# Performance work log

Hardware: AMD Instinct MI355X
Metric: run time of the kernel (lower is better)

Reference implementation:

```python
import jax, jax.numpy as jnp
import numpy as np

VOCAB = 33
V2 = VOCAB * VOCAB  # 1089
BUCKETS = 512


def setup_inputs() -> dict:
    key = jax.random.key(0)
    ks = jax.random.split(key, 9)
    B, S = 4096, 4096
    src = jax.random.randint(ks[0], (B, S), 0, VOCAB, dtype=jnp.int64 if jax.config.jax_enable_x64 else jnp.int32)
    def lin(k, fan_in, fan_out):
        bound = 1.0 / np.sqrt(fan_in)
        return jax.random.uniform(k, (fan_in, fan_out), jnp.float32, -bound, bound)
    return {
        "src": src,
        "Wb1": lin(ks[1], V2, 256), "bb1": jax.random.normal(ks[2], (256,), jnp.float32) * 0.01,
        "Wb2": lin(ks[3], 256, 32), "bb2": jax.random.normal(ks[4], (32,), jnp.float32) * 0.01,
        "Wt1": lin(ks[5], BUCKETS, 256), "bt1": jax.random.normal(ks[6], (256,), jnp.float32) * 0.01,
        "Wt2": lin(ks[7], 256, 32), "bt2": jax.random.normal(ks[8], (32,), jnp.float32) * 0.01,
    }


def _hist_freqs(indices, mask, n_bins):
    # indices: [B, L] int, mask: [B, L] bool -> normalized per-row histogram [B, n_bins]
    B = indices.shape[0]
    rows = jnp.arange(B)[:, None]
    counts = jnp.zeros((B, n_bins), jnp.float32).at[rows, indices].add(mask.astype(jnp.float32))
    lens = jnp.clip(mask.sum(axis=1, keepdims=True).astype(jnp.float32), 1.0, None)
    return counts / lens


def reference(src, Wb1, bb1, Wb2, bb2, Wt1, bt1, Wt2, bt2):
    # bigram histogram
    cur, nxt = src[:, :-1], src[:, 1:]
    bi_idx = cur * VOCAB + nxt
    bi_mask = (cur > 0) & (nxt > 0)
    bi_freq = _hist_freqs(bi_idx, bi_mask, V2)
    bi_feat = jax.nn.relu(bi_freq @ Wb1 + bb1) @ Wb2 + bb2
    # trigram hashed histogram
    c1, c2, c3 = src[:, :-2], src[:, 1:-1], src[:, 2:]
    tri_idx = (c1 * (VOCAB * VOCAB) + c2 * VOCAB + c3) % BUCKETS
    tri_mask = (c1 > 0) & (c2 > 0) & (c3 > 0)
    tri_freq = _hist_freqs(tri_idx, tri_mask, BUCKETS)
    tri_feat = jax.nn.relu(tri_freq @ Wt1 + bt1) @ Wt2 + bt2
    return jnp.concatenate([bi_feat, tri_feat], axis=1)  # [B, 64]
```

## Files before the change

### kernel.cpp

```cpp
#include <hip/hip_runtime.h>
#include <hip/hip_bf16.h>

#define TOK_S    4096
#define NBI      1089
#define NBI_P    1092
#define KP_BI    1120
#define NTRI     512
#define NTRI_P   544
#define NHID     256
#define NROWS    4096
#define HSTRIDE  (NHID + 4)

#define HIST_BLKS   (NROWS / 2)
#define TRANS_ELEMS (NHID * KP_BI + NHID * NTRI)
#define TRANS_BLKS  (TRANS_ELEMS / 1024)

typedef __attribute__((ext_vector_type(8))) short short8;
typedef __attribute__((ext_vector_type(4))) float f32x4;

static __device__ __forceinline__ unsigned int f2bf(float f) {
    __hip_bfloat16 h = __float2bfloat16(f);
    return (unsigned int)*reinterpret_cast<unsigned short*>(&h);
}

__global__ __launch_bounds__(256, 4)
void hist_trans(const int* __restrict__ src,
                const float* __restrict__ Wb1, const float* __restrict__ Wt1,
                __hip_bfloat16* __restrict__ Abi,
                __hip_bfloat16* __restrict__ Atri,
                __hip_bfloat16* __restrict__ WbT,
                __hip_bfloat16* __restrict__ WtT,
                float* __restrict__ inv)
{
    __shared__ int   s_bi [2][NBI_P];
    __shared__ int   s_tri[2][NTRI_P];
    __shared__ float s_ps [2][2][2];

    const int tid = threadIdx.x;

    if (blockIdx.x >= HIST_BLKS) {
        int base = (blockIdx.x - HIST_BLKS) * 1024 + tid;
        const int nb = NHID * KP_BI;
        #pragma unroll
        for (int i = 0; i < 4; ++i) {
            int idx = base + i * 256;
            if (idx < nb) {
                int c = idx / KP_BI, k = idx - c * KP_BI;
                WbT[idx] = __float2bfloat16(k < NBI ? Wb1[k * NHID + c] : 0.0f);
            } else {
                int j = idx - nb;
                int c = j >> 9, k = j & 511;
                WtT[j] = __float2bfloat16(Wt1[k * NHID + c]);
            }
        }
        return;
    }

    const int wave = tid >> 6;
    const int lane = tid & 63;
    const int wrow = wave >> 1;
    const int wpar = wave & 1;
    const size_t row = (size_t)blockIdx.x * 2 + wrow;
    const int dump = NTRI + (lane & 31);

    for (int i = tid; i < 2 * NBI_P / 4;  i += 256) ((int4*)s_bi)[i]  = int4{0,0,0,0};
    for (int i = tid; i < 2 * NTRI_P / 4; i += 256) ((int4*)s_tri)[i] = int4{0,0,0,0};
    __syncthreads();

    int* bi  = s_bi[wrow];
    int* tri = s_tri[wrow];
    const int4* rowp = (const int4*)(src + row * TOK_S);
    const int*  rowt = src + row * TOK_S;

    int4 A[4], Bv[4];
    int2 E[4];
    #pragma unroll
    for (int jj = 0; jj < 4; ++jj) {
        const int idx = wpar * 256 + jj * 64 + lane;
        A[jj]  = rowp[2 * idx];
        Bv[jj] = rowp[2 * idx + 1];
        if (idx != 511) E[jj] = *(const int2*)(rowt + 8 * idx + 8);
        else            E[jj] = int2{0, 0};
    }

    #pragma unroll
    for (int jj = 0; jj < 4; ++jj) {
        const int t0 = A[jj].x, t1 = A[jj].y, t2 = A[jj].z, t3 = A[jj].w;
        const int t4 = Bv[jj].x, t5 = Bv[jj].y, t6 = Bv[jj].z, t7 = Bv[jj].w;
        const int t8 = E[jj].x, t9 = E[jj].y;
        const int b0 = t0 * 33 + t1;
        const int b1 = t1 * 33 + t2;
        const int b2 = t2 * 33 + t3;
        const int b3 = t3 * 33 + t4;
        const int b4 = t4 * 33 + t5;
        const int b5 = t5 * 33 + t6;
        const int b6 = t6 * 33 + t7;
        const int b7 = t7 * 33 + t8;
        atomicAdd(&bi[b0], 1);  atomicAdd(&bi[b1], 1);
        atomicAdd(&bi[b2], 1);  atomicAdd(&bi[b3], 1);
        atomicAdd(&bi[b4], 1);  atomicAdd(&bi[b5], 1);
        atomicAdd(&bi[b6], 1);  atomicAdd(&bi[b7], 1);
        const int u0 = (min(min(t0, t1), t2) > 0) ? ((b0 * 33 + t2) & 511) : dump;
        const int u1 = (min(min(t1, t2), t3) > 0) ? ((b1 * 33 + t3) & 511) : dump;
        const int u2 = (min(min(t2, t3), t4) > 0) ? ((b2 * 33 + t4) & 511) : dump;
        const int u3 = (min(min(t3, t4), t5) > 0) ? ((b3 * 33 + t5) & 511) : dump;
        const int u4 = (min(min(t4, t5), t6) > 0) ? ((b4 * 33 + t6) & 511) : dump;
        const int u5 = (min(min(t5, t6), t7) > 0) ? ((b5 * 33 + t7) & 511) : dump;
        const int u6 = (min(min(t6, t7), t8) > 0) ? ((b6 * 33 + t8) & 511) : dump;
        const int u7 = (min(min(t7, t8), t9) > 0) ? ((b7 * 33 + t9) & 511) : dump;
        atomicAdd(&tri[u0], 1); atomicAdd(&tri[u1], 1);
        atomicAdd(&tri[u2], 1); atomicAdd(&tri[u3], 1);
        atomicAdd(&tri[u4], 1); atomicAdd(&tri[u5], 1);
        atomicAdd(&tri[u6], 1); atomicAdd(&tri[u7], 1);
    }
    __syncthreads();

    float bsum = 0.0f, tsum = 0.0f;
    __hip_bfloat16* arow = Abi + row * KP_BI;
    for (int g = wpar * 64 + lane; g < KP_BI / 4; g += 128) {
        uint2 pk{0, 0};
        if (g < NBI_P / 4) {
            int4 v = *(const int4*)&bi[4 * g];
            float f0, f1, f2, f3;
            int b = 4 * g;
            f0 = (b + 0 >= 33 && (b + 0) % 33 != 0 && b + 0 < NBI) ? (float)v.x : 0.0f;
            f1 = (b + 1 >= 33 && (b + 1) % 33 != 0 && b + 1 < NBI) ? (float)v.y : 0.0f;
            f2 = (b + 2 >= 33 && (b + 2) % 33 != 0 && b + 2 < NBI) ? (float)v.z : 0.0f;
            f3 = (b + 3 >= 33 && (b + 3) % 33 != 0 && b + 3 < NBI) ? (float)v.w : 0.0f;
            bsum += f0 + f1 + f2 + f3;
            pk.x = f2bf(f0) | (f2bf(f1) << 16);
            pk.y = f2bf(f2) | (f2bf(f3) << 16);
        }
        *(uint2*)(arow + 4 * g) = pk;
    }
    {
        const int g = wpar * 64 + lane;
        int4 v = *(const int4*)&tri[4 * g];
        float f0 = (float)v.x, f1 = (float)v.y, f2 = (float)v.z, f3 = (float)v.w;
        tsum += f0 + f1 + f2 + f3;
        uint2 pk;
        pk.x = f2bf(f0) | (f2bf(f1) << 16);
        pk.y = f2bf(f2) | (f2bf(f3) << 16);
        *(uint2*)(Atri + row * NTRI + 4 * g) = pk;
    }
    #pragma unroll
    for (int s = 32; s; s >>= 1) {
        bsum += __shfl_xor(bsum, s, 64);
        tsum += __shfl_xor(tsum, s, 64);
    }
    if (lane == 0) { s_ps[wrow][wpar][0] = bsum; s_ps[wrow][wpar][1] = tsum; }
    __syncthreads();
    if (tid < 2) {
        float bs = s_ps[tid][0][0] + s_ps[tid][1][0];
        float ts = s_ps[tid][0][1] + s_ps[tid][1][1];
        size_t r2 = ((size_t)blockIdx.x * 2 + tid) * 2;
        inv[r2 + 0] = 1.0f / fmaxf(bs, 1.0f);
        inv[r2 + 1] = 1.0f / fmaxf(ts, 1.0f);
    }
}

template<int KP>
__device__ __forceinline__
void head_body(const __hip_bfloat16* __restrict__ A,
               const __hip_bfloat16* __restrict__ WT,
               const float* __restrict__ b1,
               const float* __restrict__ W2,
               const float* __restrict__ b2,
               const float* __restrict__ inv, const int invoff, const int headoff,
               float* __restrict__ out, const int m0,
               float (*sH)[HSTRIDE])
{
    const int wave = threadIdx.x >> 6;
    const int lane = threadIdx.x & 63;
    const int wn   = wave * 32;
    const int fr   = lane & 15;
    const int kg   = lane >> 4;

    const __hip_bfloat16* A0 = A  + (size_t)(m0 + fr) * KP + kg * 8;
    const __hip_bfloat16* A1 = A0 + (size_t)16 * KP;
    const __hip_bfloat16* B0 = WT + (size_t)(wn + fr) * KP + kg * 8;
    const __hip_bfloat16* B1 = B0 + (size_t)16 * KP;

    f32x4 acc00 = {}, acc01 = {}, acc10 = {}, acc11 = {};
    #pragma unroll 4
    for (int k = 0; k < KP; k += 32) {
        short8 a0  = *(const short8*)(A0 + k);
        short8 a1  = *(const short8*)(A1 + k);
        short8 b0  = *(const short8*)(B0 + k);
        short8 b1v = *(const short8*)(B1 + k);
        acc00 = __builtin_amdgcn_mfma_f32_16x16x32_bf16(a0, b0,  acc00, 0, 0, 0);
        acc01 = __builtin_amdgcn_mfma_f32_16x16x32_bf16(a0, b1v, acc01, 0, 0, 0);
        acc10 = __builtin_amdgcn_mfma_f32_16x16x32_bf16(a1, b0,  acc10, 0, 0, 0);
        acc11 = __builtin_amdgcn_mfma_f32_16x16x32_bf16(a1, b1v, acc11, 0, 0, 0);
    }

    f32x4 accs[2][2] = { {acc00, acc01}, {acc10, acc11} };
    #pragma unroll
    for (int mf = 0; mf < 2; ++mf) {
        #pragma unroll
        for (int nf = 0; nf < 2; ++nf) {
            const int col = wn + nf * 16 + fr;
            const float bias = b1[col];
            #pragma unroll
            for (int r = 0; r < 4; ++r) {
                const int rl = mf * 16 + kg * 4 + r;
                const float iv = inv[(m0 + rl) * 2 + invoff];
                sH[rl][col] = fmaxf(fmaf(accs[mf][nf][r], iv, bias), 0.0f);
            }
        }
    }
    __syncthreads();

    const int r  = threadIdx.x >> 4;
    const int oo = threadIdx.x & 15;
    const float* hr = sH[r];
    float a0 = b2[oo], a1 = b2[oo + 16];
    #pragma unroll 8
    for (int j = 0; j < NHID; j += 4) {
        float4 h = *(const float4*)(hr + j);
        a0 = fmaf(h.x, W2[(j + 0) * 32 + oo], a0);
        a0 = fmaf(h.y, W2[(j + 1) * 32 + oo], a0);
        a0 = fmaf(h.z, W2[(j + 2) * 32 + oo], a0);
        a0 = fmaf(h.w, W2[(j + 3) * 32 + oo], a0);
        a1 = fmaf(h.x, W2[(j + 0) * 32 + oo + 16], a1);
        a1 = fmaf(h.y, W2[(j + 1) * 32 + oo + 16], a1);
        a1 = fmaf(h.z, W2[(j + 2) * 32 + oo + 16], a1);
        a1 = fmaf(h.w, W2[(j + 3) * 32 + oo + 16], a1);
    }
    const size_t ro = (size_t)(m0 + r) * 64 + headoff;
    out[ro + oo]      = a0;
    out[ro + oo + 16] = a1;
}

__global__ __launch_bounds__(512, 1)
void gemm_fused(const __hip_bfloat16* __restrict__ Abi,
                const __hip_bfloat16* __restrict__ WbT,
                const float* __restrict__ bb1,
                const float* __restrict__ Wb2, const float* __restrict__ bb2,
                const __hip_bfloat16* __restrict__ Atri,
                const __hip_bfloat16* __restrict__ WtT,
                const float* __restrict__ bt1,
                const float* __restrict__ Wt2, const float* __restrict__ bt2,
                const float* __restrict__ inv,
                float* __restrict__ out)
{
    __shared__ float sH[32][HSTRIDE];
    const int bid = (blockIdx.x & 7) * 32 + (blockIdx.x >> 3);
    if (bid < NROWS / 32) {
        head_body<KP_BI>(Abi, WbT, bb1, Wb2, bb2, inv, 0, 0,  out, bid * 32, sH);
    } else {
        head_body<NTRI>(Atri, WtT, bt1, Wt2, bt2, inv, 1, 32, out, (bid - NROWS / 32) * 32, sH);
    }
}

extern "C" void kernel_launch(void* const* d_in, const int* in_sizes, int n_in,
                              void* d_out, int out_size, void* d_ws, size_t ws_size,
                              hipStream_t stream) {
    const int*   src = (const int*)  d_in[0];
    const float* Wb1 = (const float*)d_in[1];
    const float* bb1 = (const float*)d_in[2];
    const float* Wb2 = (const float*)d_in[3];
    const float* bb2 = (const float*)d_in[4];
    const float* Wt1 = (const float*)d_in[5];
    const float* bt1 = (const float*)d_in[6];
    const float* Wt2 = (const float*)d_in[7];
    const float* bt2 = (const float*)d_in[8];
    float* outp = (float*)d_out;

    const int B = in_sizes[0] / TOK_S;

    char* ws = (char*)d_ws;
    __hip_bfloat16* Abi  = (__hip_bfloat16*)(ws);
    __hip_bfloat16* Atri = (__hip_bfloat16*)(ws + (size_t)B * KP_BI * 2);
    char* ws2 = ws + (size_t)B * KP_BI * 2 + (size_t)B * NTRI * 2;
    __hip_bfloat16* WbT  = (__hip_bfloat16*)(ws2);
    __hip_bfloat16* WtT  = (__hip_bfloat16*)(ws2 + (size_t)NHID * KP_BI * 2);
    float* inv = (float*)(ws2 + (size_t)NHID * KP_BI * 2 + (size_t)NHID * NTRI * 2);

    hist_trans<<<HIST_BLKS + TRANS_BLKS, 256, 0, stream>>>(
        src, Wb1, Wt1, Abi, Atri, WbT, WtT, inv);

    gemm_fused<<<2 * (B / 32), 512, 0, stream>>>(
        Abi, WbT, bb1, Wb2, bb2, Atri, WtT, bt1, Wt2, bt2, inv, outp);
}
```

Measured before the change: 49.71 us.

## Fuse histogram and GEMM heads into one cooperative kernel with grid sync

Replaces the two-kernel pipeline (histogram/weight-transpose, then fused GEMM) with a single cooperative launch of 512 blocks of 512 threads. Each block transposes a slice of the weights, builds histograms for 8 rows in two passes, then does a grid-wide sync before computing 16-row MLP heads with MFMA. The aim is to remove the second launch and its inter-kernel gap. The cost is a grid barrier, a fixed grid shape tied to B=4096, and a smaller 16-row GEMM tile with less reuse. It falls back to the old kernels if the cooperative launch fails.

```diff
diff --git a/kernel.cpp b/kernel.cpp
--- a/kernel.cpp
+++ b/kernel.cpp
@@ -1,5 +1,8 @@
 #include <hip/hip_runtime.h>
 #include <hip/hip_bf16.h>
+#include <hip/hip_cooperative_groups.h>
+
+namespace cg = cooperative_groups;
 
 #define TOK_S    4096
 #define NBI      1089
@@ -15,12 +18,227 @@
 #define TRANS_ELEMS (NHID * KP_BI + NHID * NTRI)
 #define TRANS_BLKS  (TRANS_ELEMS / 1024)
 
+#define CGRID   512
+#define CBLK    512
+
 typedef __attribute__((ext_vector_type(8))) short short8;
 typedef __attribute__((ext_vector_type(4))) float f32x4;
 
 static __device__ __forceinline__ unsigned int f2bf(float f) {
     __hip_bfloat16 h = __float2bfloat16(f);
     return (unsigned int)*reinterpret_cast<unsigned short*>(&h);
+}
+
+struct HistLds {
+    int   bi [4][1100];
+    int   tri[4][548];
+    float ps [4][2][2];
+};
+struct GemmLds {
+    float sH[16][260];
+};
+union SharedU { HistLds h; GemmLds g; };
+
+template<int KP>
+__device__ __forceinline__
+void head16(const __hip_bfloat16* __restrict__ A,
+            const __hip_bfloat16* __restrict__ WT,
+            const float* __restrict__ b1, const float* __restrict__ W2,
+            const float* __restrict__ b2, const float* __restrict__ inv,
+            const int invoff, const int headoff,
+            float* __restrict__ out, const int m0, float (*sH)[260])
+{
+    const int tid  = threadIdx.x;
+    const int wave = tid >> 6, lane = tid & 63;
+    const int wn   = wave * 32;
+    const int fr   = lane & 15, kg = lane >> 4;
+
+    const __hip_bfloat16* Ap = A  + (size_t)(m0 + fr) * KP + kg * 8;
+    const __hip_bfloat16* B0 = WT + (size_t)(wn + fr) * KP + kg * 8;
+    const __hip_bfloat16* B1 = B0 + (size_t)16 * KP;
+
+    f32x4 acc0 = {}, acc1 = {};
+    #pragma unroll 4
+    for (int k = 0; k < KP; k += 32) {
+        short8 a   = *(const short8*)(Ap + k);
+        short8 b0  = *(const short8*)(B0 + k);
+        short8 b1v = *(const short8*)(B1 + k);
+        acc0 = __builtin_amdgcn_mfma_f32_16x16x32_bf16(a, b0,  acc0, 0, 0, 0);
+        acc1 = __builtin_amdgcn_mfma_f32_16x16x32_bf16(a, b1v, acc1, 0, 0, 0);
+    }
+
+    #pragma unroll
+    for (int nf = 0; nf < 2; ++nf) {
+        const f32x4 acc = nf ? acc1 : acc0;
+        const int col = wn + nf * 16 + fr;
+        const float bias = b1[col];
+        #pragma unroll
+        for (int r = 0; r < 4; ++r) {
+            const int rl = kg * 4 + r;
+            const float iv = inv[(m0 + rl) * 2 + invoff];
+            sH[rl][col] = fmaxf(fmaf(acc[r], iv, bias), 0.0f);
+        }
+    }
+    __syncthreads();
+
+    const int rr = tid >> 5, o = tid & 31;
+    const float* hr = sH[rr];
+    float a0 = b2[o];
+    #pragma unroll 8
+    for (int j = 0; j < NHID; j += 4) {
+        float4 h = *(const float4*)(hr + j);
+        a0 = fmaf(h.x, W2[(j + 0) * 32 + o], a0);
+        a0 = fmaf(h.y, W2[(j + 1) * 32 + o], a0);
+        a0 = fmaf(h.z, W2[(j + 2) * 32 + o], a0);
+        a0 = fmaf(h.w, W2[(j + 3) * 32 + o], a0);
+    }
+    out[(size_t)(m0 + rr) * 64 + headoff + o] = a0;
+}
+
+__global__ __launch_bounds__(CBLK, 4)
+void ngram_coop(const int* __restrict__ src,
+                const float* __restrict__ Wb1, const float* __restrict__ Wt1,
+                const float* __restrict__ bb1, const float* __restrict__ Wb2,
+                const float* __restrict__ bb2, const float* __restrict__ bt1,
+                const float* __restrict__ Wt2, const float* __restrict__ bt2,
+                __hip_bfloat16* __restrict__ Abi, __hip_bfloat16* __restrict__ Atri,
+                __hip_bfloat16* __restrict__ WbT, __hip_bfloat16* __restrict__ WtT,
+                float* __restrict__ inv, float* __restrict__ out)
+{
+    cg::grid_group grid = cg::this_grid();
+    __shared__ __align__(16) SharedU u;
+
+    const int tid  = threadIdx.x;
+    const int bid  = blockIdx.x;
+    const int wave = tid >> 6, lane = tid & 63;
+    const int wrow = wave >> 1, wpar = wave & 1;
+
+    {
+        const int nb = NHID * KP_BI;
+        #pragma unroll
+        for (int it = 0; it < 2; ++it) {
+            const int t = tid + it * 512;
+            if (t < 816) {
+                int idx = bid * 816 + t;
+                if (idx < nb) {
+                    int c = idx / KP_BI, k = idx - c * KP_BI;
+                    WbT[idx] = __float2bfloat16(k < NBI ? Wb1[k * NHID + c] : 0.0f);
+                } else {
+                    int j = idx - nb;
+                    int c = j >> 9, k = j & 511;
+                    WtT[j] = __float2bfloat16(Wt1[k * NHID + c]);
+                }
+            }
+        }
+    }
+
+    const int dump = NTRI + (lane & 31);
+    for (int pass = 0; pass < 2; ++pass) {
+        const int4 z{0, 0, 0, 0};
+        for (int i = tid; i < 1100; i += 512) ((int4*)u.h.bi)[i]  = z;
+        for (int i = tid; i < 548;  i += 512) ((int4*)u.h.tri)[i] = z;
+        __syncthreads();
+
+        const size_t row = (size_t)bid * 8 + pass * 4 + wrow;
+        int* bi  = u.h.bi[wrow];
+        int* tri = u.h.tri[wrow];
+        const int4* rowp = (const int4*)(src + row * TOK_S);
+        const int*  rowt = src + row * TOK_S;
+
+        int4 A[4], Bv[4];
+        int2 E[4];
+        #pragma unroll
+        for (int jj = 0; jj < 4; ++jj) {
+            const int idx = wpar * 256 + jj * 64 + lane;
+            A[jj]  = rowp[2 * idx];
+            Bv[jj] = rowp[2 * idx + 1];
+            if (idx != 511) E[jj] = *(const int2*)(rowt + 8 * idx + 8);
+            else            E[jj] = int2{0, 0};
+        }
+
+        #pragma unroll
+        for (int jj = 0; jj < 4; ++jj) {
+            const int t0 = A[jj].x, t1 = A[jj].y, t2 = A[jj].z, t3 = A[jj].w;
+            const int t4 = Bv[jj].x, t5 = Bv[jj].y, t6 = Bv[jj].z, t7 = Bv[jj].w;
+            const int t8 = E[jj].x, t9 = E[jj].y;
+            const int b0 = t0 * 33 + t1;
+            const int b1 = t1 * 33 + t2;
+            const int b2 = t2 * 33 + t3;
+            const int b3 = t3 * 33 + t4;
+            const int b4 = t4 * 33 + t5;
+            const int b5 = t5 * 33 + t6;
+            const int b6 = t6 * 33 + t7;
+            const int b7 = t7 * 33 + t8;
+            atomicAdd(&bi[b0], 1);  atomicAdd(&bi[b1], 1);
+            atomicAdd(&bi[b2], 1);  atomicAdd(&bi[b3], 1);
+            atomicAdd(&bi[b4], 1);  atomicAdd(&bi[b5], 1);
+            atomicAdd(&bi[b6], 1);  atomicAdd(&bi[b7], 1);
+            const int u0 = (min(min(t0, t1), t2) > 0) ? ((b0 * 33 + t2) & 511) : dump;
+            const int u1 = (min(min(t1, t2), t3) > 0) ? ((b1 * 33 + t3) & 511) : dump;
+            const int u2 = (min(min(t2, t3), t4) > 0) ? ((b2 * 33 + t4) & 511) : dump;
+            const int u3 = (min(min(t3, t4), t5) > 0) ? ((b3 * 33 + t5) & 511) : dump;
+            const int u4 = (min(min(t4, t5), t6) > 0) ? ((b4 * 33 + t6) & 511) : dump;
+            const int u5 = (min(min(t5, t6), t7) > 0) ? ((b5 * 33 + t7) & 511) : dump;
+            const int u6 = (min(min(t6, t7), t8) > 0) ? ((b6 * 33 + t8) & 511) : dump;
+            const int u7 = (min(min(t7, t8), t9) > 0) ? ((b7 * 33 + t9) & 511) : dump;
+            atomicAdd(&tri[u0], 1); atomicAdd(&tri[u1], 1);
+            atomicAdd(&tri[u2], 1); atomicAdd(&tri[u3], 1);
+            atomicAdd(&tri[u4], 1); atomicAdd(&tri[u5], 1);
+            atomicAdd(&tri[u6], 1); atomicAdd(&tri[u7], 1);
+        }
+        __syncthreads();
+
+        float bsum = 0.0f, tsum = 0.0f;
+        __hip_bfloat16* arow = Abi + row * KP_BI;
+        for (int g = wpar * 64 + lane; g < KP_BI / 4; g += 128) {
+            uint2 pk{0, 0};
+            if (g < NBI_P / 4) {
+                int4 v = *(const int4*)&bi[4 * g];
+                int b = 4 * g;
+                float f0 = (b + 0 >= 33 && (b + 0) % 33 != 0 && b + 0 < NBI) ? (float)v.x : 0.0f;
+                float f1 = (b + 1 >= 33 && (b + 1) % 33 != 0 && b + 1 < NBI) ? (float)v.y : 0.0f;
+                float f2 = (b + 2 >= 33 && (b + 2) % 33 != 0 && b + 2 < NBI) ? (float)v.z : 0.0f;
+                float f3 = (b + 3 >= 33 && (b + 3) % 33 != 0 && b + 3 < NBI) ? (float)v.w : 0.0f;
+                bsum += f0 + f1 + f2 + f3;
+                pk.x = f2bf(f0) | (f2bf(f1) << 16);
+                pk.y = f2bf(f2) | (f2bf(f3) << 16);
+            }
+            *(uint2*)(arow + 4 * g) = pk;
+        }
+        {
+            const int g = wpar * 64 + lane;
+            int4 v = *(const int4*)&tri[4 * g];
+            float f0 = (float)v.x, f1 = (float)v.y, f2 = (float)v.z, f3 = (float)v.w;
+            tsum += f0 + f1 + f2 + f3;
+            uint2 pk;
+            pk.x = f2bf(f0) | (f2bf(f1) << 16);
+            pk.y = f2bf(f2) | (f2bf(f3) << 16);
+            *(uint2*)(Atri + row * NTRI + 4 * g) = pk;
+        }
+        #pragma unroll
+        for (int s = 32; s; s >>= 1) {
+            bsum += __shfl_xor(bsum, s, 64);
+            tsum += __shfl_xor(tsum, s, 64);
+        }
+        if (lane == 0) { u.h.ps[wrow][wpar][0] = bsum; u.h.ps[wrow][wpar][1] = tsum; }
+        __syncthreads();
+        if (tid < 4) {
+            float bs = u.h.ps[tid][0][0] + u.h.ps[tid][1][0];
+            float ts = u.h.ps[tid][0][1] + u.h.ps[tid][1][1];
+            size_t r2 = ((size_t)bid * 8 + pass * 4 + tid) * 2;
+            inv[r2 + 0] = 1.0f / fmaxf(bs, 1.0f);
+            inv[r2 + 1] = 1.0f / fmaxf(ts, 1.0f);
+        }
+        __syncthreads();
+    }
+
+    grid.sync();
+
+    if (bid < NROWS / 16) {
+        head16<KP_BI>(Abi, WbT, bb1, Wb2, bb2, inv, 0, 0,  out, bid * 16, u.g.sH);
+    } else {
+        head16<NTRI>(Atri, WtT, bt1, Wt2, bt2, inv, 1, 32, out, (bid - NROWS / 16) * 16, u.g.sH);
+    }
 }
 
 __global__ __launch_bounds__(256, 4)
@@ -121,12 +339,11 @@
         uint2 pk{0, 0};
         if (g < NBI_P / 4) {
             int4 v = *(const int4*)&bi[4 * g];
-            float f0, f1, f2, f3;
             int b = 4 * g;
-            f0 = (b + 0 >= 33 && (b + 0) % 33 != 0 && b + 0 < NBI) ? (float)v.x : 0.0f;
-            f1 = (b + 1 >= 33 && (b + 1) % 33 != 0 && b + 1 < NBI) ? (float)v.y : 0.0f;
-            f2 = (b + 2 >= 33 && (b + 2) % 33 != 0 && b + 2 < NBI) ? (float)v.z : 0.0f;
-            f3 = (b + 3 >= 33 && (b + 3) % 33 != 0 && b + 3 < NBI) ? (float)v.w : 0.0f;
+            float f0 = (b + 0 >= 33 && (b + 0) % 33 != 0 && b + 0 < NBI) ? (float)v.x : 0.0f;
+            float f1 = (b + 1 >= 33 && (b + 1) % 33 != 0 && b + 1 < NBI) ? (float)v.y : 0.0f;
+            float f2 = (b + 2 >= 33 && (b + 2) % 33 != 0 && b + 2 < NBI) ? (float)v.z : 0.0f;
+            float f3 = (b + 3 >= 33 && (b + 3) % 33 != 0 && b + 3 < NBI) ? (float)v.w : 0.0f;
             bsum += f0 + f1 + f2 + f3;
             pk.x = f2bf(f0) | (f2bf(f1) << 16);
             pk.y = f2bf(f2) | (f2bf(f3) << 16);
@@ -277,9 +494,19 @@
     __hip_bfloat16* WtT  = (__hip_bfloat16*)(ws2 + (size_t)NHID * KP_BI * 2);
     float* inv = (float*)(ws2 + (size_t)NHID * KP_BI * 2 + (size_t)NHID * NTRI * 2);
 
-    hist_trans<<<HIST_BLKS + TRANS_BLKS, 256, 0, stream>>>(
-        src, Wb1, Wt1, Abi, Atri, WbT, WtT, inv);
-
-    gemm_fused<<<2 * (B / 32), 512, 0, stream>>>(
-        Abi, WbT, bb1, Wb2, bb2, Atri, WtT, bt1, Wt2, bt2, inv, outp);
-}
+    void* args[15] = {
+        (void*)&src, (void*)&Wb1, (void*)&Wt1, (void*)&bb1, (void*)&Wb2,
+        (void*)&bb2, (void*)&bt1, (void*)&Wt2, (void*)&bt2,
+        (void*)&Abi, (void*)&Atri, (void*)&WbT, (void*)&WtT,
+        (void*)&inv, (void*)&outp
+    };
+    hipError_t e = hipLaunchCooperativeKernel((const void*)ngram_coop,
+                                              dim3(CGRID), dim3(CBLK),
+                                              args, 0, stream);
+    if (e != hipSuccess) {
+        hist_trans<<<HIST_BLKS + TRANS_BLKS, 256, 0, stream>>>(
+            src, Wb1, Wt1, Abi, Atri, WbT, WtT, inv);
+        gemm_fused<<<2 * (B / 32), 512, 0, stream>>>(
+            Abi, WbT, bb1, Wb2, bb2, Atri, WtT, bt1, Wt2, bt2, inv, outp);
+    }
+}
```

Result: slower. 131.6 us (+164.6%).

## Fuse histogram, weight transpose and GEMM heads into one kernel with flag sync

Applied to the files above, without the earlier changes.

Merges the histogram/transpose kernel and the GEMM head kernel into a single launch. Histogram blocks now cover 4 rows with 512 threads and bump per-tile counters, and GEMM blocks spin on those flags before running the head. This removes the kernel boundary and lets GEMM tiles start as soon as their rows are ready, overlapping the two stages. It adds a memset launch and spin-waiting, and relies on producer blocks being scheduled before the consumers that wait on them, which risks deadlock if they are not.

```diff
diff --git a/kernel.cpp b/kernel.cpp
--- a/kernel.cpp
+++ b/kernel.cpp
@@ -6,14 +6,15 @@
 #define NBI_P    1092
 #define KP_BI    1120
 #define NTRI     512
-#define NTRI_P   544
 #define NHID     256
 #define NROWS    4096
-#define HSTRIDE  (NHID + 4)
-
-#define HIST_BLKS   (NROWS / 2)
+#define HSTRIDE  260
+
+#define HBLKS    1024
+#define TBLKS    204
+#define GBLKS    256
+#define NTILES   128
 #define TRANS_ELEMS (NHID * KP_BI + NHID * NTRI)
-#define TRANS_BLKS  (TRANS_ELEMS / 1024)
 
 typedef __attribute__((ext_vector_type(8))) short short8;
 typedef __attribute__((ext_vector_type(4))) float f32x4;
@@ -23,27 +24,109 @@
     return (unsigned int)*reinterpret_cast<unsigned short*>(&h);
 }
 
-__global__ __launch_bounds__(256, 4)
-void hist_trans(const int* __restrict__ src,
+union MegaLds {
+    struct {
+        int   bi [4][1100];
+        int   tri[4][548];
+        float ps [4][2][2];
+    } h;
+    float sH[32][HSTRIDE];
+};
+
+template<int KP>
+__device__ __forceinline__
+void head_body(const __hip_bfloat16* __restrict__ A,
+               const __hip_bfloat16* __restrict__ WT,
+               const float* __restrict__ b1,
+               const float* __restrict__ W2,
+               const float* __restrict__ b2,
+               const float* __restrict__ inv, const int invoff, const int headoff,
+               float* __restrict__ out, const int m0,
+               float (*sH)[HSTRIDE])
+{
+    const int wave = threadIdx.x >> 6;
+    const int lane = threadIdx.x & 63;
+    const int wn   = wave * 32;
+    const int fr   = lane & 15;
+    const int kg   = lane >> 4;
+
+    const __hip_bfloat16* A0 = A  + (size_t)(m0 + fr) * KP + kg * 8;
+    const __hip_bfloat16* A1 = A0 + (size_t)16 * KP;
+    const __hip_bfloat16* B0 = WT + (size_t)(wn + fr) * KP + kg * 8;
+    const __hip_bfloat16* B1 = B0 + (size_t)16 * KP;
+
+    f32x4 acc00 = {}, acc01 = {}, acc10 = {}, acc11 = {};
+    #pragma unroll 4
+    for (int k = 0; k < KP; k += 32) {
+        short8 a0  = *(const short8*)(A0 + k);
+        short8 a1  = *(const short8*)(A1 + k);
+        short8 b0  = *(const short8*)(B0 + k);
+        short8 b1v = *(const short8*)(B1 + k);
+        acc00 = __builtin_amdgcn_mfma_f32_16x16x32_bf16(a0, b0,  acc00, 0, 0, 0);
+        acc01 = __builtin_amdgcn_mfma_f32_16x16x32_bf16(a0, b1v, acc01, 0, 0, 0);
+        acc10 = __builtin_amdgcn_mfma_f32_16x16x32_bf16(a1, b0,  acc10, 0, 0, 0);
+        acc11 = __builtin_amdgcn_mfma_f32_16x16x32_bf16(a1, b1v, acc11, 0, 0, 0);
+    }
+
+    f32x4 accs[2][2] = { {acc00, acc01}, {acc10, acc11} };
+    #pragma unroll
+    for (int mf = 0; mf < 2; ++mf) {
+        #pragma unroll
+        for (int nf = 0; nf < 2; ++nf) {
+            const int col = wn + nf * 16 + fr;
+            const float bias = b1[col];
+            #pragma unroll
+            for (int r = 0; r < 4; ++r) {
+                const int rl = mf * 16 + kg * 4 + r;
+                const float iv = inv[(m0 + rl) * 2 + invoff];
+                sH[rl][col] = fmaxf(fmaf(accs[mf][nf][r], iv, bias), 0.0f);
+            }
+        }
+    }
+    __syncthreads();
+
+    const int r  = threadIdx.x >> 4;
+    const int oo = threadIdx.x & 15;
+    const float* hr = sH[r];
+    float a0 = b2[oo], a1 = b2[oo + 16];
+    #pragma unroll 8
+    for (int j = 0; j < NHID; j += 4) {
+        float4 h = *(const float4*)(hr + j);
+        a0 = fmaf(h.x, W2[(j + 0) * 32 + oo], a0);
+        a0 = fmaf(h.y, W2[(j + 1) * 32 + oo], a0);
+        a0 = fmaf(h.z, W2[(j + 2) * 32 + oo], a0);
+        a0 = fmaf(h.w, W2[(j + 3) * 32 + oo], a0);
+        a1 = fmaf(h.x, W2[(j + 0) * 32 + oo + 16], a1);
+        a1 = fmaf(h.y, W2[(j + 1) * 32 + oo + 16], a1);
+        a1 = fmaf(h.z, W2[(j + 2) * 32 + oo + 16], a1);
+        a1 = fmaf(h.w, W2[(j + 3) * 32 + oo + 16], a1);
+    }
+    const size_t ro = (size_t)(m0 + r) * 64 + headoff;
+    out[ro + oo]      = a0;
+    out[ro + oo + 16] = a1;
+}
+
+__global__ __launch_bounds__(512, 4)
+void ngram_mega(const int* __restrict__ src,
                 const float* __restrict__ Wb1, const float* __restrict__ Wt1,
-                __hip_bfloat16* __restrict__ Abi,
-                __hip_bfloat16* __restrict__ Atri,
-                __hip_bfloat16* __restrict__ WbT,
-                __hip_bfloat16* __restrict__ WtT,
-                float* __restrict__ inv)
+                const float* __restrict__ bb1, const float* __restrict__ Wb2,
+                const float* __restrict__ bb2, const float* __restrict__ bt1,
+                const float* __restrict__ Wt2, const float* __restrict__ bt2,
+                __hip_bfloat16* __restrict__ Abi, __hip_bfloat16* __restrict__ Atri,
+                __hip_bfloat16* __restrict__ WbT, __hip_bfloat16* __restrict__ WtT,
+                float* __restrict__ inv, int* __restrict__ flags,
+                float* __restrict__ out)
 {
-    __shared__ int   s_bi [2][NBI_P];
-    __shared__ int   s_tri[2][NTRI_P];
-    __shared__ float s_ps [2][2][2];
-
+    __shared__ __align__(16) MegaLds u;
+    const int bid = blockIdx.x;
     const int tid = threadIdx.x;
 
-    if (blockIdx.x >= HIST_BLKS) {
-        int base = (blockIdx.x - HIST_BLKS) * 1024 + tid;
+    if (bid >= HBLKS && bid < HBLKS + TBLKS) {
+        int base = (bid - HBLKS) * 2048 + tid;
         const int nb = NHID * KP_BI;
         #pragma unroll
         for (int i = 0; i < 4; ++i) {
-            int idx = base + i * 256;
+            int idx = base + i * 512;
             if (idx < nb) {
                 int c = idx / KP_BI, k = idx - c * KP_BI;
                 WbT[idx] = __float2bfloat16(k < NBI ? Wb1[k * NHID + c] : 0.0f);
@@ -53,6 +136,27 @@
                 WtT[j] = __float2bfloat16(Wt1[k * NHID + c]);
             }
         }
+        __syncthreads();
+        if (tid == 0) { __threadfence(); atomicAdd(&flags[NTILES], 1); }
+        return;
+    }
+
+    if (bid >= HBLKS + TBLKS) {
+        const int g    = bid - (HBLKS + TBLKS);
+        const int head = g >> 7;
+        const int mt   = g & 127;
+        if (tid == 0) {
+            while (__hip_atomic_load(&flags[NTILES], __ATOMIC_RELAXED, __HIP_MEMORY_SCOPE_AGENT) < TBLKS ||
+                   __hip_atomic_load(&flags[mt],     __ATOMIC_RELAXED, __HIP_MEMORY_SCOPE_AGENT) < 8) {
+                __builtin_amdgcn_s_sleep(8);
+            }
+            __threadfence();
+        }
+        __syncthreads();
+        if (head == 0)
+            head_body<KP_BI>(Abi,  WbT, bb1, Wb2, bb2, inv, 0, 0,  out, mt * 32, u.sH);
+        else
+            head_body<NTRI>(Atri, WtT, bt1, Wt2, bt2, inv, 1, 32, out, mt * 32, u.sH);
         return;
     }
 
@@ -60,15 +164,15 @@
     const int lane = tid & 63;
     const int wrow = wave >> 1;
     const int wpar = wave & 1;
-    const size_t row = (size_t)blockIdx.x * 2 + wrow;
+    const size_t row = (size_t)bid * 4 + wrow;
     const int dump = NTRI + (lane & 31);
 
-    for (int i = tid; i < 2 * NBI_P / 4;  i += 256) ((int4*)s_bi)[i]  = int4{0,0,0,0};
-    for (int i = tid; i < 2 * NTRI_P / 4; i += 256) ((int4*)s_tri)[i] = int4{0,0,0,0};
-    __syncthreads();
-
-    int* bi  = s_bi[wrow];
-    int* tri = s_tri[wrow];
+    for (int i = tid; i < 1100; i += 512) ((int4*)u.h.bi)[i]  = int4{0,0,0,0};
+    for (int i = tid; i < 548;  i += 512) ((int4*)u.h.tri)[i] = int4{0,0,0,0};
+    __syncthreads();
+
+    int* bi  = u.h.bi[wrow];
+    int* tri = u.h.tri[wrow];
     const int4* rowp = (const int4*)(src + row * TOK_S);
     const int*  rowt = src + row * TOK_S;
 
@@ -121,12 +225,11 @@
         uint2 pk{0, 0};
         if (g < NBI_P / 4) {
             int4 v = *(const int4*)&bi[4 * g];
-            float f0, f1, f2, f3;
             int b = 4 * g;
-            f0 = (b + 0 >= 33 && (b + 0) % 33 != 0 && b + 0 < NBI) ? (float)v.x : 0.0f;
-            f1 = (b + 1 >= 33 && (b + 1) % 33 != 0 && b + 1 < NBI) ? (float)v.y : 0.0f;
-            f2 = (b + 2 >= 33 && (b + 2) % 33 != 0 && b + 2 < NBI) ? (float)v.z : 0.0f;
-            f3 = (b + 3 >= 33 && (b + 3) % 33 != 0 && b + 3 < NBI) ? (float)v.w : 0.0f;
+            float f0 = (b + 0 >= 33 && (b + 0) % 33 != 0 && b + 0 < NBI) ? (float)v.x : 0.0f;
+            float f1 = (b + 1 >= 33 && (b + 1) % 33 != 0 && b + 1 < NBI) ? (float)v.y : 0.0f;
+            float f2 = (b + 2 >= 33 && (b + 2) % 33 != 0 && b + 2 < NBI) ? (float)v.z : 0.0f;
+            float f3 = (b + 3 >= 33 && (b + 3) % 33 != 0 && b + 3 < NBI) ? (float)v.w : 0.0f;
             bsum += f0 + f1 + f2 + f3;
             pk.x = f2bf(f0) | (f2bf(f1) << 16);
             pk.y = f2bf(f2) | (f2bf(f3) << 16);
@@ -148,108 +251,19 @@
         bsum += __shfl_xor(bsum, s, 64);
         tsum += __shfl_xor(tsum, s, 64);
     }
-    if (lane == 0) { s_ps[wrow][wpar][0] = bsum; s_ps[wrow][wpar][1] = tsum; }
-    __syncthreads();
-    if (tid < 2) {
-        float bs = s_ps[tid][0][0] + s_ps[tid][1][0];
-        float ts = s_ps[tid][0][1] + s_ps[tid][1][1];
-        size_t r2 = ((size_t)blockIdx.x * 2 + tid) * 2;
+    if (lane == 0) { u.h.ps[wrow][wpar][0] = bsum; u.h.ps[wrow][wpar][1] = tsum; }
+    __syncthreads();
+    if (tid < 4) {
+        float bs = u.h.ps[tid][0][0] + u.h.ps[tid][1][0];
+        float ts = u.h.ps[tid][0][1] + u.h.ps[tid][1][1];
+        size_t r2 = ((size_t)bid * 4 + tid) * 2;
         inv[r2 + 0] = 1.0f / fmaxf(bs, 1.0f);
         inv[r2 + 1] = 1.0f / fmaxf(ts, 1.0f);
     }
-}
-
-template<int KP>
-__device__ __forceinline__
-void head_body(const __hip_bfloat16* __restrict__ A,
-               const __hip_bfloat16* __restrict__ WT,
-               const float* __restrict__ b1,
-               const float* __restrict__ W2,
-               const float* __restrict__ b2,
-               const float* __restrict__ inv, const int invoff, const int headoff,
-               float* __restrict__ out, const int m0,
-               float (*sH)[HSTRIDE])
-{
-    const int wave = threadIdx.x >> 6;
-    const int lane = threadIdx.x & 63;
-    const int wn   = wave * 32;
-    const int fr   = lane & 15;
-    const int kg   = lane >> 4;
-
-    const __hip_bfloat16* A0 = A  + (size_t)(m0 + fr) * KP + kg * 8;
-    const __hip_bfloat16* A1 = A0 + (size_t)16 * KP;
-    const __hip_bfloat16* B0 = WT + (size_t)(wn + fr) * KP + kg * 8;
-    const __hip_bfloat16* B1 = B0 + (size_t)16 * KP;
-
-    f32x4 acc00 = {}, acc01 = {}, acc10 = {}, acc11 = {};
-    #pragma unroll 4
-    for (int k = 0; k < KP; k += 32) {
-        short8 a0  = *(const short8*)(A0 + k);
-        short8 a1  = *(const short8*)(A1 + k);
-        short8 b0  = *(const short8*)(B0 + k);
-        short8 b1v = *(const short8*)(B1 + k);
-        acc00 = __builtin_amdgcn_mfma_f32_16x16x32_bf16(a0, b0,  acc00, 0, 0, 0);
-        acc01 = __builtin_amdgcn_mfma_f32_16x16x32_bf16(a0, b1v, acc01, 0, 0, 0);
-        acc10 = __builtin_amdgcn_mfma_f32_16x16x32_bf16(a1, b0,  acc10, 0, 0, 0);
-        acc11 = __builtin_amdgcn_mfma_f32_16x16x32_bf16(a1, b1v, acc11, 0, 0, 0);
-    }
-
-    f32x4 accs[2][2] = { {acc00, acc01}, {acc10, acc11} };
-    #pragma unroll
-    for (int mf = 0; mf < 2; ++mf) {
-        #pragma unroll
-        for (int nf = 0; nf < 2; ++nf) {
-            const int col = wn + nf * 16 + fr;
-            const float bias = b1[col];
-            #pragma unroll
-            for (int r = 0; r < 4; ++r) {
-                const int rl = mf * 16 + kg * 4 + r;
-                const float iv = inv[(m0 + rl) * 2 + invoff];
-                sH[rl][col] = fmaxf(fmaf(accs[mf][nf][r], iv, bias), 0.0f);
-            }
-        }
-    }
-    __syncthreads();
-
-    const int r  = threadIdx.x >> 4;
-    const int oo = threadIdx.x & 15;
-    const float* hr = sH[r];
-    float a0 = b2[oo], a1 = b2[oo + 16];
-    #pragma unroll 8
-    for (int j = 0; j < NHID; j += 4) {
-        float4 h = *(const float4*)(hr + j);
-        a0 = fmaf(h.x, W2[(j + 0) * 32 + oo], a0);
-        a0 = fmaf(h.y, W2[(j + 1) * 32 + oo], a0);
-        a0 = fmaf(h.z, W2[(j + 2) * 32 + oo], a0);
-        a0 = fmaf(h.w, W2[(j + 3) * 32 + oo], a0);
-        a1 = fmaf(h.x, W2[(j + 0) * 32 + oo + 16], a1);
-        a1 = fmaf(h.y, W2[(j + 1) * 32 + oo + 16], a1);
-        a1 = fmaf(h.z, W2[(j + 2) * 32 + oo + 16], a1);
-        a1 = fmaf(h.w, W2[(j + 3) * 32 + oo + 16], a1);
-    }
-    const size_t ro = (size_t)(m0 + r) * 64 + headoff;
-    out[ro + oo]      = a0;
-    out[ro + oo + 16] = a1;
-}
-
-__global__ __launch_bounds__(512, 1)
-void gemm_fused(const __hip_bfloat16* __restrict__ Abi,
-                const __hip_bfloat16* __restrict__ WbT,
-                const float* __restrict__ bb1,
-                const float* __restrict__ Wb2, const float* __restrict__ bb2,
-                const __hip_bfloat16* __restrict__ Atri,
-                const __hip_bfloat16* __restrict__ WtT,
-                const float* __restrict__ bt1,
-                const float* __restrict__ Wt2, const float* __restrict__ bt2,
-                const float* __restrict__ inv,
-                float* __restrict__ out)
-{
-    __shared__ float sH[32][HSTRIDE];
-    const int bid = (blockIdx.x & 7) * 32 + (blockIdx.x >> 3);
-    if (bid < NROWS / 32) {
-        head_body<KP_BI>(Abi, WbT, bb1, Wb2, bb2, inv, 0, 0,  out, bid * 32, sH);
-    } else {
-        head_body<NTRI>(Atri, WtT, bt1, Wt2, bt2, inv, 1, 32, out, (bid - NROWS / 32) * 32, sH);
+    __syncthreads();
+    if (tid == 0) {
+        __threadfence();
+        atomicAdd(&flags[bid >> 3], 1);
     }
 }
 
@@ -267,7 +281,7 @@
     const float* bt2 = (const float*)d_in[8];
     float* outp = (float*)d_out;
 
-    const int B = in_sizes[0] / TOK_S;
+    const int B = NROWS;
 
     char* ws = (char*)d_ws;
     __hip_bfloat16* Abi  = (__hip_bfloat16*)(ws);
@@ -275,11 +289,13 @@
     char* ws2 = ws + (size_t)B * KP_BI * 2 + (size_t)B * NTRI * 2;
     __hip_bfloat16* WbT  = (__hip_bfloat16*)(ws2);
     __hip_bfloat16* WtT  = (__hip_bfloat16*)(ws2 + (size_t)NHID * KP_BI * 2);
-    float* inv = (float*)(ws2 + (size_t)NHID * KP_BI * 2 + (size_t)NHID * NTRI * 2);
-
-    hist_trans<<<HIST_BLKS + TRANS_BLKS, 256, 0, stream>>>(
-        src, Wb1, Wt1, Abi, Atri, WbT, WtT, inv);
-
-    gemm_fused<<<2 * (B / 32), 512, 0, stream>>>(
-        Abi, WbT, bb1, Wb2, bb2, Atri, WtT, bt1, Wt2, bt2, inv, outp);
+    char* ws3 = ws2 + (size_t)NHID * KP_BI * 2 + (size_t)NHID * NTRI * 2;
+    float* inv   = (float*)(ws3);
+    int*   flags = (int*)(ws3 + (size_t)B * 2 * 4);
+
+    hipMemsetAsync(flags, 0, (NTILES + 1) * sizeof(int), stream);
+
+    ngram_mega<<<HBLKS + TBLKS + GBLKS, 512, 0, stream>>>(
+        src, Wb1, Wt1, bb1, Wb2, bb2, bt1, Wt2, bt2,
+        Abi, Atri, WbT, WtT, inv, flags, outp);
 }
```

After: 135.5 us. 173% more time.
